# Performance work log

Hardware: AMD Instinct MI355X
Metric: run time of the kernel (lower is better)

Reference implementation:

```python
import jax, jax.numpy as jnp
import numpy as np

B, S, D, H, E, O = 8, 2048, 512, 8, 64, 512  # batch, seq, d_in, heads, head_dim, out_dim
NEG_INF = -1e9  # keras Attention adds -1e9 to masked scores


def setup_inputs() -> dict:
    key = jax.random.key(0)
    kq, kk, kv, ko, kx = jax.random.split(key, 5)
    # glorot-uniform-style scale for kernel_size=1 convs (fan_in=D, fan_out=E)
    sqkv = float(np.sqrt(6.0 / (D + E)))
    so = float(np.sqrt(6.0 / (H * E + O)))
    return {
        "query": jax.random.normal(kx, (B, S, D), dtype=jnp.float32),
        "Wq": jax.random.uniform(kq, (H, D, E), jnp.float32, -sqkv, sqkv),
        "Wk": jax.random.uniform(kk, (H, D, E), jnp.float32, -sqkv, sqkv),
        "Wv": jax.random.uniform(kv, (H, D, E), jnp.float32, -sqkv, sqkv),
        "Wo": jax.random.uniform(ko, (H * E, O), jnp.float32, -so, so),
    }


def reference(query, Wq, Wk, Wv, Wo):
    # value defaults to query (self-attention). Conv1D(kernel_size=1, no bias)
    # is a per-timestep linear map; all heads batched into one einsum.
    Q = jnp.einsum('bsd,hde->bhse', query, Wq)
    K = jnp.einsum('bsd,hde->bhse', query, Wk)
    V = jnp.einsum('bsd,hde->bhse', query, Wv)
    # keras Attention(use_scale=False, causal=True): scores = Q K^T (no scale)
    scores = jnp.einsum('bhse,bhte->bhst', Q, K)
    causal = jnp.tril(jnp.ones((S, S), dtype=bool))  # [S, S]
    scores = jnp.where(causal, scores, NEG_INF)
    attn = jax.nn.softmax(scores, axis=-1)
    ctx = jnp.einsum('bhst,bhte->bhse', attn, V)  # [B, H, S, E]
    # concat heads along last axis (head-major), then 1x1 conv projection
    ctx = ctx.transpose(0, 2, 1, 3).reshape(B, S, H * E)
    return jnp.einsum('bsf,fo->bso', ctx, Wo)
```

## Files before the change

kernel.cpp:

```cpp
#include <hip/hip_runtime.h>
#include <stdint.h>

#define Bb 8
#define Ss 2048
#define Dd 512
#define Hh 8
#define Ee 64
#define Oo 512
#define Ff 512
#define Ncat 1536

typedef _Float16 half_t;
typedef __attribute__((ext_vector_type(8))) _Float16 f16x8;
typedef __attribute__((ext_vector_type(4))) float f32x4;
typedef __attribute__((ext_vector_type(16))) float f32x16;
typedef __attribute__((ext_vector_type(4))) float f4;
typedef __attribute__((ext_vector_type(4))) half_t h16x4;
typedef __attribute__((ext_vector_type(4))) unsigned int u32x4;

__device__ __forceinline__ float exp2_fast(float x) {
    float r; asm("v_exp_f32 %0, %1" : "=v"(r) : "v"(x)); return r;
}
__device__ __forceinline__ f32x16 zero16() {
    f32x16 z;
#pragma unroll
    for (int i = 0; i < 16; ++i) z[i] = 0.f;
    return z;
}
__device__ __forceinline__ void gload16(const half_t* g, half_t* l) {
    __builtin_amdgcn_global_load_lds(
        (const __attribute__((address_space(1))) void*)g,
        (__attribute__((address_space(3))) void*)l, 16, 0, 0);
}

__global__ __launch_bounds__(256) void k_cvt_x(const float* __restrict__ x,
                                               half_t* __restrict__ xh) {
    int t = blockIdx.x * 256 + threadIdx.x;
    int s = t >> 6, c = t & 63;
    int cg = c >> 3, cl = c & 7;
    const float* src = x + (size_t)s * Dd + c * 8;
    f4 v0 = *(const f4*)src;
    f4 v1 = *(const f4*)(src + 4);
    union { half_t h[8]; u32x4 u; } o;
#pragma unroll
    for (int j = 0; j < 4; ++j) { o.h[j] = (half_t)v0[j]; o.h[4 + j] = (half_t)v1[j]; }
    int cd = cg * 8 + (cl ^ (s & 7));
    *(u32x4*)(xh + (size_t)s * Dd + cd * 8) = o.u;
}

__global__ __launch_bounds__(256) void k_cvt_w(const float* __restrict__ Wq, const float* __restrict__ Wk,
                                               const float* __restrict__ Wv, const float* __restrict__ Wo,
                                               half_t* __restrict__ Wcat, half_t* __restrict__ WoT) {
    int t = blockIdx.x * 256 + threadIdx.x;
    union { half_t h[8]; u32x4 u; } o;
    if (t < Ncat * 64) {
        int n = t >> 6, dc = t & 63;
        int sel = n >> 9, h = (n >> 6) & 7, e = n & 63;
        const float* W = (sel == 0) ? Wq : (sel == 1) ? Wk : Wv;
        const float* src = W + ((size_t)h * Dd + dc * 8) * Ee + e;
#pragma unroll
        for (int j = 0; j < 8; ++j) o.h[j] = (half_t)src[(size_t)j * Ee];
        int dcs = (dc & ~7) | ((dc & 7) ^ (n & 7));
        *(u32x4*)(Wcat + (size_t)n * Dd + dcs * 8) = o.u;
    } else {
        int u2 = t - Ncat * 64;
        int oo = u2 >> 6, fc = u2 & 63;
        const float* src = Wo + (size_t)(fc * 8) * Oo + oo;
#pragma unroll
        for (int j = 0; j < 8; ++j) o.h[j] = (half_t)src[(size_t)j * Oo];
        int fcs = (fc & ~7) | ((fc & 7) ^ (oo & 7));
        *(u32x4*)(WoT + (size_t)oo * Ff + fcs * 8) = o.u;
    }
}

__global__ __launch_bounds__(256, 2) void k_qkv(const half_t* __restrict__ A,
                                                const half_t* __restrict__ Bw,
                                                half_t* __restrict__ Q,
                                                half_t* __restrict__ K,
                                                half_t* __restrict__ Vt) {
    __shared__ __attribute__((aligned(16))) half_t Ab[2][128 * 64];
    __shared__ __attribute__((aligned(16))) half_t Bbuf[2][128 * 64];

    int bid = blockIdx.x;
    int virt = (bid & 7) * 192 + (bid >> 3);
    int bm = virt / 12, bn = virt % 12;
    int m0 = bm * 128, n0 = bn * 128;

    int wave = threadIdx.x >> 6, lane = threadIdx.x & 63;
    int ar = lane & 15, kg = lane >> 4;
    int wm = wave >> 1, wn = wave & 1;
    int lr = lane >> 3, lc = lane & 7;

    f32x4 acc[4][4];
#pragma unroll
    for (int i = 0; i < 4; ++i)
#pragma unroll
        for (int j = 0; j < 4; ++j) acc[i][j] = (f32x4){0, 0, 0, 0};

#define STAGE_QKV(buf, kt)                                                              \
    {                                                                                   \
        _Pragma("unroll")                                                               \
        for (int i = 0; i < 4; ++i) {                                                   \
            int seg = wave * 4 + i;                                                     \
            int row = seg * 8 + lr;                                                     \
            gload16(A  + (size_t)(m0 + row) * Dd + (kt) * 64 + lc * 8, &Ab[buf][seg * 512]);   \
            gload16(Bw + (size_t)(n0 + row) * Dd + (kt) * 64 + lc * 8, &Bbuf[buf][seg * 512]); \
        }                                                                               \
    }

    STAGE_QKV(0, 0);
    __syncthreads();
    int cur = 0;
    for (int kt = 0; kt < 8; ++kt) {
        if (kt < 7) STAGE_QKV(cur ^ 1, kt + 1);
        f16x8 bf[4][2];
#pragma unroll
        for (int n = 0; n < 4; ++n) {
            int row = wn * 64 + n * 16 + ar;
#pragma unroll
            for (int kh = 0; kh < 2; ++kh)
                bf[n][kh] = *(const f16x8*)&Bbuf[cur][row * 64 + (((kg + kh * 4)) ^ (row & 7)) * 8];
        }
#pragma unroll
        for (int mi = 0; mi < 4; ++mi) {
            int row = wm * 64 + mi * 16 + ar;
            f16x8 a0 = *(const f16x8*)&Ab[cur][row * 64 + ((kg)     ^ (row & 7)) * 8];
            f16x8 a1 = *(const f16x8*)&Ab[cur][row * 64 + ((kg + 4) ^ (row & 7)) * 8];
#pragma unroll
            for (int n = 0; n < 4; ++n) {
                acc[mi][n] = __builtin_amdgcn_mfma_f32_16x16x32_f16(a0, bf[n][0], acc[mi][n], 0, 0, 0);
                acc[mi][n] = __builtin_amdgcn_mfma_f32_16x16x32_f16(a1, bf[n][1], acc[mi][n], 0, 0, 0);
            }
        }
        __syncthreads();
        cur ^= 1;
    }
    int sel = n0 >> 9;
#pragma unroll
    for (int sn = 0; sn < 4; ++sn) {
        int nb = n0 + wn * 64 + sn * 16;
        int h = (nb >> 6) & 7, eb = nb & 63;
#pragma unroll
        for (int mi = 0; mi < 4; ++mi)
#pragma unroll
            for (int r = 0; r < 4; ++r) {
                int sg = m0 + wm * 64 + mi * 16 + kg * 4 + r;
                int bh = (sg >> 11) * 8 + h, sl = sg & 2047;
                half_t val = (half_t)acc[mi][sn][r];
                if (sel == 0)      Q [((size_t)bh * Ss + sl) * Ee + eb + ar] = val;
                else if (sel == 1) K [((size_t)bh * Ss + sl) * Ee + eb + ar] = val;
                else               Vt[((size_t)bh * Ee + eb + ar) * Ss + sl] = val;
            }
    }
#undef STAGE_QKV
}

__global__ __launch_bounds__(256, 4) void k_attn(const half_t* __restrict__ Q,
                                                 const half_t* __restrict__ Kg,
                                                 const half_t* __restrict__ Vtg,
                                                 half_t* __restrict__ ctx) {
    __shared__ __attribute__((aligned(16))) half_t Klds[2][32 * 64];
    __shared__ __attribute__((aligned(16))) half_t Vlds[2][64 * 32];

    int bid = blockIdx.x;
    int xcd = bid & 7;
    int idx = bid >> 3;
    int qb  = 15 - (idx >> 3);
    int bh  = xcd * 8 + (idx & 7);

    int wave = threadIdx.x >> 6, lane = threadIdx.x & 63;
    int ql = lane & 31, hi = lane >> 5;
    int qt32 = qb * 4 + wave;
    int ktmax = qb * 4 + 3;
    int qg = qt32 * 32 + ql;

    const half_t* Qb = Q   + (size_t)bh * Ss * Ee;
    const half_t* Kb = Kg  + (size_t)bh * Ss * Ee;
    const half_t* Vb = Vtg + (size_t)bh * Ee * Ss;

    const half_t* qp = Qb + (size_t)qg * Ee + hi * 8;
    f16x8 qf[4];
    const half_t l2e = (half_t)1.44269504f;
#pragma unroll
    for (int d = 0; d < 4; ++d) {
        qf[d] = *(const f16x8*)(qp + d * 16);
#pragma unroll
        for (int j = 0; j < 8; ++j) qf[d][j] *= l2e;
    }

    f32x16 ot0 = zero16(), ot1 = zero16();
    float m = -1e30f, lp = 0.f;

    const half_t* KbSrc = Kb + (size_t)(lane & 31) * Ee + (2 * wave + (lane >> 5)) * 8;
    const half_t* VbSrc = Vb + ((size_t)((wave >> 1) * 32 + (lane & 31))) * Ss
                             + (2 * (wave & 1) + (lane >> 5)) * 8;

#define STAGE_KV(buf, kt)                                            \
    {                                                                \
        gload16(KbSrc + (size_t)(kt) * 32 * Ee, &Klds[buf][wave * 512]); \
        gload16(VbSrc + (kt) * 32,              &Vlds[buf][wave * 512]); \
    }

    STAGE_KV(0, 0);
    int cur = 0;
    for (int kt = 0; kt <= ktmax; ++kt) {
        __syncthreads();
        if (kt < ktmax) STAGE_KV(cur ^ 1, kt + 1);
        if (kt <= qt32) {
            f16x8 kf0 = *(const f16x8*)&Klds[cur][lane * 8];
            f16x8 kf1 = *(const f16x8*)&Klds[cur][512 + lane * 8];
            f16x8 kf2 = *(const f16x8*)&Klds[cur][1024 + lane * 8];
            f16x8 kf3 = *(const f16x8*)&Klds[cur][1536 + lane * 8];

            f32x16 s = zero16();
            __builtin_amdgcn_s_setprio(1);
            s = __builtin_amdgcn_mfma_f32_32x32x16_f16(kf0, qf[0], s, 0, 0, 0);
            s = __builtin_amdgcn_mfma_f32_32x32x16_f16(kf1, qf[1], s, 0, 0, 0);
            s = __builtin_amdgcn_mfma_f32_32x32x16_f16(kf2, qf[2], s, 0, 0, 0);
            s = __builtin_amdgcn_mfma_f32_32x32x16_f16(kf3, qf[3], s, 0, 0, 0);
            __builtin_amdgcn_s_setprio(0);

            if (kt == qt32) {
#pragma unroll
                for (int r = 0; r < 16; ++r) {
                    int kloc = (r & 3) + 8 * (r >> 2) + 4 * hi;
                    if (kloc > ql) s[r] = -1e30f;
                }
            }

            float mt = s[0];
#pragma unroll
            for (int r = 1; r < 16; ++r) mt = fmaxf(mt, s[r]);
            mt = fmaxf(mt, __shfl_xor(mt, 32));
            if (!__all(mt <= m + 8.0f)) {
                float mn = fmaxf(m, mt);
                float sc = exp2_fast(m - mn);
#pragma unroll
                for (int r = 0; r < 16; ++r) { ot0[r] *= sc; ot1[r] *= sc; }
                lp *= sc;
                m = mn;
            }
            float rs = 0.f;
#pragma unroll
            for (int r = 0; r < 16; ++r) { s[r] = exp2_fast(s[r] - m); rs += s[r]; }
            lp += rs;

            unsigned w[8];
#pragma unroll
            for (int mm = 0; mm < 8; ++mm)
                asm("v_cvt_pkrtz_f16_f32 %0, %1, %2" : "=v"(w[mm]) : "v"(s[2 * mm]), "v"(s[2 * mm + 1]));
            unsigned t0 = (unsigned)__shfl_xor((int)(hi ? w[0] : w[2]), 32);
            unsigned t1 = (unsigned)__shfl_xor((int)(hi ? w[1] : w[3]), 32);
            unsigned t2 = (unsigned)__shfl_xor((int)(hi ? w[4] : w[6]), 32);
            unsigned t3 = (unsigned)__shfl_xor((int)(hi ? w[5] : w[7]), 32);
            union { unsigned u[4]; f16x8 v; } pb0, pb1;
            pb0.u[0] = hi ? t0 : w[0];  pb0.u[1] = hi ? t1 : w[1];
            pb0.u[2] = hi ? w[2] : t0;  pb0.u[3] = hi ? w[3] : t1;
            pb1.u[0] = hi ? t2 : w[4];  pb1.u[1] = hi ? t3 : w[5];
            pb1.u[2] = hi ? w[6] : t2;  pb1.u[3] = hi ? w[7] : t3;

            f16x8 va00 = *(const f16x8*)&Vlds[cur][lane * 8];
            f16x8 va01 = *(const f16x8*)&Vlds[cur][512 + lane * 8];
            f16x8 va10 = *(const f16x8*)&Vlds[cur][1024 + lane * 8];
            f16x8 va11 = *(const f16x8*)&Vlds[cur][1536 + lane * 8];

            __builtin_amdgcn_s_setprio(1);
            ot0 = __builtin_amdgcn_mfma_f32_32x32x16_f16(va00, pb0.v, ot0, 0, 0, 0);
            ot0 = __builtin_amdgcn_mfma_f32_32x32x16_f16(va01, pb1.v, ot0, 0, 0, 0);
            ot1 = __builtin_amdgcn_mfma_f32_32x32x16_f16(va10, pb0.v, ot1, 0, 0, 0);
            ot1 = __builtin_amdgcn_mfma_f32_32x32x16_f16(va11, pb1.v, ot1, 0, 0, 0);
            __builtin_amdgcn_s_setprio(0);
        }
        cur ^= 1;
    }
#undef STAGE_KV

    float lf = lp + __shfl_xor(lp, 32);
    float inv = 1.0f / lf;
    int b = bh >> 3, h = bh & 7;
    int qs = qg & 7;
    half_t* cb = ctx + ((size_t)b * Ss + qg) * Ff;
#pragma unroll
    for (int g = 0; g < 4; ++g) {
        h16x4 v0, v1;
#pragma unroll
        for (int j = 0; j < 4; ++j) {
            v0[j] = (half_t)(ot0[g * 4 + j] * inv);
            v1[j] = (half_t)(ot1[g * 4 + j] * inv);
        }
        *(h16x4*)(cb + (h * 8 + (g ^ qs)) * 8 + 4 * hi)       = v0;
        *(h16x4*)(cb + (h * 8 + ((g + 4) ^ qs)) * 8 + 4 * hi) = v1;
    }
}

__global__ __launch_bounds__(256, 2) void k_proj(const half_t* __restrict__ A,
                                                 const half_t* __restrict__ Bw,
                                                 float* __restrict__ out) {
    __shared__ __attribute__((aligned(16))) half_t Ab[2][128 * 64];
    __shared__ __attribute__((aligned(16))) half_t Bbuf[2][128 * 64];

    int bid = blockIdx.x;
    int virt = (bid & 7) * 64 + (bid >> 3);
    int bm = virt >> 2, bn = virt & 3;
    int m0 = bm * 128, n0 = bn * 128;

    int wave = threadIdx.x >> 6, lane = threadIdx.x & 63;
    int ar = lane & 15, kg = lane >> 4;
    int wm = wave >> 1, wn = wave & 1;
    int lr = lane >> 3, lc = lane & 7;

    f32x4 acc[4][4];
#pragma unroll
    for (int i = 0; i < 4; ++i)
#pragma unroll
        for (int j = 0; j < 4; ++j) acc[i][j] = (f32x4){0, 0, 0, 0};

#define STAGE_PRJ(buf, kt)                                                              \
    {                                                                                   \
        _Pragma("unroll")                                                               \
        for (int i = 0; i < 4; ++i) {                                                   \
            int seg = wave * 4 + i;                                                     \
            int row = seg * 8 + lr;                                                     \
            gload16(A  + (size_t)(m0 + row) * Ff + (kt) * 64 + lc * 8, &Ab[buf][seg * 512]);   \
            gload16(Bw + (size_t)(n0 + row) * Ff + (kt) * 64 + lc * 8, &Bbuf[buf][seg * 512]); \
        }                                                                               \
    }

    STAGE_PRJ(0, 0);
    __syncthreads();
    int cur = 0;
    for (int kt = 0; kt < 8; ++kt) {
        if (kt < 7) STAGE_PRJ(cur ^ 1, kt + 1);
        f16x8 bf[4][2];
#pragma unroll
        for (int n = 0; n < 4; ++n) {
            int row = wn * 64 + n * 16 + ar;
#pragma unroll
            for (int kh = 0; kh < 2; ++kh)
                bf[n][kh] = *(const f16x8*)&Bbuf[cur][row * 64 + (((kg + kh * 4)) ^ (row & 7)) * 8];
        }
#pragma unroll
        for (int mi = 0; mi < 4; ++mi) {
            int row = wm * 64 + mi * 16 + ar;
            f16x8 a0 = *(const f16x8*)&Ab[cur][row * 64 + ((kg)     ^ (row & 7)) * 8];
            f16x8 a1 = *(const f16x8*)&Ab[cur][row * 64 + ((kg + 4) ^ (row & 7)) * 8];
#pragma unroll
            for (int n = 0; n < 4; ++n) {
                acc[mi][n] = __builtin_amdgcn_mfma_f32_16x16x32_f16(a0, bf[n][0], acc[mi][n], 0, 0, 0);
                acc[mi][n] = __builtin_amdgcn_mfma_f32_16x16x32_f16(a1, bf[n][1], acc[mi][n], 0, 0, 0);
            }
        }
        __syncthreads();
        cur ^= 1;
    }
#pragma unroll
    for (int sn = 0; sn < 4; ++sn)
#pragma unroll
        for (int mi = 0; mi < 4; ++mi)
#pragma unroll
            for (int r = 0; r < 4; ++r) {
                int sg = m0 + wm * 64 + mi * 16 + kg * 4 + r;
                out[(size_t)sg * Oo + n0 + wn * 64 + sn * 16 + ar] = acc[mi][sn][r];
            }
#undef STAGE_PRJ
}

extern "C" void kernel_launch(void* const* d_in, const int* in_sizes, int n_in,
                              void* d_out, int out_size, void* d_ws, size_t ws_size,
                              hipStream_t stream) {
    const float* x  = (const float*)d_in[0];
    const float* Wq = (const float*)d_in[1];
    const float* Wk = (const float*)d_in[2];
    const float* Wv = (const float*)d_in[3];
    const float* Wo = (const float*)d_in[4];
    float* out = (float*)d_out;

    char* ws = (char*)d_ws;
    size_t off = 0;
    half_t* xh   = (half_t*)(ws + off); off += (size_t)Bb * Ss * Dd * 2;
    half_t* Wcat = (half_t*)(ws + off); off += (size_t)Ncat * Dd * 2;
    half_t* WoT  = (half_t*)(ws + off); off += (size_t)Oo * Ff * 2;
    half_t* Qd   = (half_t*)(ws + off); off += (size_t)Bb * Hh * Ss * Ee * 2;
    half_t* Kd   = (half_t*)(ws + off); off += (size_t)Bb * Hh * Ss * Ee * 2;
    half_t* Vtd  = (half_t*)(ws + off); off += (size_t)Bb * Hh * Ss * Ee * 2;
    half_t* ctx  = (half_t*)(ws + off); off += (size_t)Bb * Ss * Ff * 2;

    k_cvt_x<<<4096, 256, 0, stream>>>(x, xh);
    k_cvt_w<<<512, 256, 0, stream>>>(Wq, Wk, Wv, Wo, Wcat, WoT);
    k_qkv<<<1536, 256, 0, stream>>>(xh, Wcat, Qd, Kd, Vtd);
    k_attn<<<1024, 256, 0, stream>>>(Qd, Kd, Vtd, ctx);
    k_proj<<<512, 256, 0, stream>>>(ctx, WoT, out);
}
```

Measured before the change: 157.7 us.

## Stage 64-key tiles per barrier and reorder causal query-block dispatch

The attention kernel now stages 64 keys per double-buffer step instead of 32, doubling K/V LDS buffers and processing two 32-key subtiles per synchronization to halve barrier count. Query-block scheduling changes from strictly descending to an interleaved pattern to balance causal work across waves of blocks. The row-max reduction is rewritten as a tree for shorter dependency chains. It costs more LDS per block, which may reduce occupancy, and loads some keys that masked waves skip.

```diff
diff --git a/kernel.cpp b/kernel.cpp
--- a/kernel.cpp
+++ b/kernel.cpp
@@ -159,19 +159,26 @@
                                                  const half_t* __restrict__ Kg,
                                                  const half_t* __restrict__ Vtg,
                                                  half_t* __restrict__ ctx) {
-    __shared__ __attribute__((aligned(16))) half_t Klds[2][32 * 64];
-    __shared__ __attribute__((aligned(16))) half_t Vlds[2][64 * 32];
+    __shared__ __attribute__((aligned(16))) half_t Klds[2][64 * 64];
+    __shared__ __attribute__((aligned(16))) half_t Vlds[2][64 * 64];
 
     int bid = blockIdx.x;
     int xcd = bid & 7;
     int idx = bid >> 3;
-    int qb  = 15 - (idx >> 3);
+    int g   = idx >> 3;
+    int g0 = g & 3, j = g >> 2;
+    int qb;
+    switch (j) {
+        case 0:  qb = 15 - g0; break;
+        case 1:  qb = 8 + (g0 ^ 2); break;
+        case 2:  qb = 4 + g0; break;
+        default: qb = g0 ^ 1; break;
+    }
     int bh  = xcd * 8 + (idx & 7);
 
     int wave = threadIdx.x >> 6, lane = threadIdx.x & 63;
     int ql = lane & 31, hi = lane >> 5;
     int qt32 = qb * 4 + wave;
-    int ktmax = qb * 4 + 3;
     int qg = qt32 * 32 + ql;
 
     const half_t* Qb = Q   + (size_t)bh * Ss * Ee;
@@ -185,91 +192,106 @@
     for (int d = 0; d < 4; ++d) {
         qf[d] = *(const f16x8*)(qp + d * 16);
 #pragma unroll
-        for (int j = 0; j < 8; ++j) qf[d][j] *= l2e;
+        for (int jj = 0; jj < 8; ++jj) qf[d][jj] *= l2e;
     }
 
     f32x16 ot0 = zero16(), ot1 = zero16();
     float m = -1e30f, lp = 0.f;
 
-    const half_t* KbSrc = Kb + (size_t)(lane & 31) * Ee + (2 * wave + (lane >> 5)) * 8;
-    const half_t* VbSrc = Vb + ((size_t)((wave >> 1) * 32 + (lane & 31))) * Ss
-                             + (2 * (wave & 1) + (lane >> 5)) * 8;
-
-#define STAGE_KV(buf, kt)                                            \
-    {                                                                \
-        gload16(KbSrc + (size_t)(kt) * 32 * Ee, &Klds[buf][wave * 512]); \
-        gload16(VbSrc + (kt) * 32,              &Vlds[buf][wave * 512]); \
+#define STAGE_KV(buf, kt64)                                                                 \
+    {                                                                                       \
+        _Pragma("unroll")                                                                   \
+        for (int c = 0; c < 2; ++c) {                                                       \
+            int seg = 2 * wave + c;                                                         \
+            int tK = seg >> 2, dK = seg & 3;                                                \
+            gload16(Kb + ((size_t)(kt64) * 64 + tK * 32 + ql) * Ee + dK * 16 + hi * 8,      \
+                    &Klds[buf][seg * 512]);                                                 \
+            int eh = (seg >> 1) & 1, d2 = seg & 1;                                          \
+            gload16(Vb + (size_t)(eh * 32 + ql) * Ss + (kt64) * 64 + tK * 32 + d2 * 16 + hi * 8, \
+                    &Vlds[buf][seg * 512]);                                                 \
+        }                                                                                   \
     }
 
     STAGE_KV(0, 0);
     int cur = 0;
-    for (int kt = 0; kt <= ktmax; ++kt) {
+    int ktmax64 = qb * 2 + 1;
+    for (int kt64 = 0; kt64 <= ktmax64; ++kt64) {
         __syncthreads();
-        if (kt < ktmax) STAGE_KV(cur ^ 1, kt + 1);
-        if (kt <= qt32) {
-            f16x8 kf0 = *(const f16x8*)&Klds[cur][lane * 8];
-            f16x8 kf1 = *(const f16x8*)&Klds[cur][512 + lane * 8];
-            f16x8 kf2 = *(const f16x8*)&Klds[cur][1024 + lane * 8];
-            f16x8 kf3 = *(const f16x8*)&Klds[cur][1536 + lane * 8];
-
-            f32x16 s = zero16();
-            __builtin_amdgcn_s_setprio(1);
-            s = __builtin_amdgcn_mfma_f32_32x32x16_f16(kf0, qf[0], s, 0, 0, 0);
-            s = __builtin_amdgcn_mfma_f32_32x32x16_f16(kf1, qf[1], s, 0, 0, 0);
-            s = __builtin_amdgcn_mfma_f32_32x32x16_f16(kf2, qf[2], s, 0, 0, 0);
-            s = __builtin_amdgcn_mfma_f32_32x32x16_f16(kf3, qf[3], s, 0, 0, 0);
-            __builtin_amdgcn_s_setprio(0);
-
-            if (kt == qt32) {
-#pragma unroll
-                for (int r = 0; r < 16; ++r) {
-                    int kloc = (r & 3) + 8 * (r >> 2) + 4 * hi;
-                    if (kloc > ql) s[r] = -1e30f;
+        if (kt64 < ktmax64) STAGE_KV(cur ^ 1, kt64 + 1);
+#pragma unroll
+        for (int st = 0; st < 2; ++st) {
+            int kt32 = kt64 * 2 + st;
+            if (kt32 <= qt32) {
+                const half_t* Kbase = &Klds[cur][st * 2048];
+                const half_t* Vbase = &Vlds[cur][st * 2048];
+                f16x8 kf0 = *(const f16x8*)&Kbase[lane * 8];
+                f16x8 kf1 = *(const f16x8*)&Kbase[512 + lane * 8];
+                f16x8 kf2 = *(const f16x8*)&Kbase[1024 + lane * 8];
+                f16x8 kf3 = *(const f16x8*)&Kbase[1536 + lane * 8];
+
+                f32x16 s = zero16();
+                __builtin_amdgcn_s_setprio(1);
+                s = __builtin_amdgcn_mfma_f32_32x32x16_f16(kf0, qf[0], s, 0, 0, 0);
+                s = __builtin_amdgcn_mfma_f32_32x32x16_f16(kf1, qf[1], s, 0, 0, 0);
+                s = __builtin_amdgcn_mfma_f32_32x32x16_f16(kf2, qf[2], s, 0, 0, 0);
+                s = __builtin_amdgcn_mfma_f32_32x32x16_f16(kf3, qf[3], s, 0, 0, 0);
+                __builtin_amdgcn_s_setprio(0);
+
+                if (kt32 == qt32) {
+#pragma unroll
+                    for (int r = 0; r < 16; ++r) {
+                        int kloc = (r & 3) + 8 * (r >> 2) + 4 * hi;
+                        if (kloc > ql) s[r] = -1e30f;
+                    }
                 }
+
+                float m0a = fmaxf(s[0], s[1]),  m1a = fmaxf(s[2], s[3]);
+                float m2a = fmaxf(s[4], s[5]),  m3a = fmaxf(s[6], s[7]);
+                float m4a = fmaxf(s[8], s[9]),  m5a = fmaxf(s[10], s[11]);
+                float m6a = fmaxf(s[12], s[13]), m7a = fmaxf(s[14], s[15]);
+                float mb0 = fmaxf(fmaxf(m0a, m1a), fmaxf(m2a, m3a));
+                float mb1 = fmaxf(fmaxf(m4a, m5a), fmaxf(m6a, m7a));
+                float mt = fmaxf(mb0, mb1);
+                mt = fmaxf(mt, __shfl_xor(mt, 32));
+                if (!__all(mt <= m + 8.0f)) {
+                    float mn = fmaxf(m, mt);
+                    float sc = exp2_fast(m - mn);
+#pragma unroll
+                    for (int r = 0; r < 16; ++r) { ot0[r] *= sc; ot1[r] *= sc; }
+                    lp *= sc;
+                    m = mn;
+                }
+                float rs = 0.f;
+#pragma unroll
+                for (int r = 0; r < 16; ++r) { s[r] = exp2_fast(s[r] - m); rs += s[r]; }
+                lp += rs;
+
+                unsigned w[8];
+#pragma unroll
+                for (int mm = 0; mm < 8; ++mm)
+                    asm("v_cvt_pkrtz_f16_f32 %0, %1, %2" : "=v"(w[mm]) : "v"(s[2 * mm]), "v"(s[2 * mm + 1]));
+                unsigned t0 = (unsigned)__shfl_xor((int)(hi ? w[0] : w[2]), 32);
+                unsigned t1 = (unsigned)__shfl_xor((int)(hi ? w[1] : w[3]), 32);
+                unsigned t2 = (unsigned)__shfl_xor((int)(hi ? w[4] : w[6]), 32);
+                unsigned t3 = (unsigned)__shfl_xor((int)(hi ? w[5] : w[7]), 32);
+                union { unsigned u[4]; f16x8 v; } pb0, pb1;
+                pb0.u[0] = hi ? t0 : w[0];  pb0.u[1] = hi ? t1 : w[1];
+                pb0.u[2] = hi ? w[2] : t0;  pb0.u[3] = hi ? w[3] : t1;
+                pb1.u[0] = hi ? t2 : w[4];  pb1.u[1] = hi ? t3 : w[5];
+                pb1.u[2] = hi ? w[6] : t2;  pb1.u[3] = hi ? w[7] : t3;
+
+                f16x8 va00 = *(const f16x8*)&Vbase[lane * 8];
+                f16x8 va01 = *(const f16x8*)&Vbase[512 + lane * 8];
+                f16x8 va10 = *(const f16x8*)&Vbase[1024 + lane * 8];
+                f16x8 va11 = *(const f16x8*)&Vbase[1536 + lane * 8];
+
+                __builtin_amdgcn_s_setprio(1);
+                ot0 = __builtin_amdgcn_mfma_f32_32x32x16_f16(va00, pb0.v, ot0, 0, 0, 0);
+                ot0 = __builtin_amdgcn_mfma_f32_32x32x16_f16(va01, pb1.v, ot0, 0, 0, 0);
+                ot1 = __builtin_amdgcn_mfma_f32_32x32x16_f16(va10, pb0.v, ot1, 0, 0, 0);
+                ot1 = __builtin_amdgcn_mfma_f32_32x32x16_f16(va11, pb1.v, ot1, 0, 0, 0);
+                __builtin_amdgcn_s_setprio(0);
             }
-
-            float mt = s[0];
-#pragma unroll
-            for (int r = 1; r < 16; ++r) mt = fmaxf(mt, s[r]);
-            mt = fmaxf(mt, __shfl_xor(mt, 32));
-            if (!__all(mt <= m + 8.0f)) {
-                float mn = fmaxf(m, mt);
-                float sc = exp2_fast(m - mn);
-#pragma unroll
-                for (int r = 0; r < 16; ++r) { ot0[r] *= sc; ot1[r] *= sc; }
-                lp *= sc;
-                m = mn;
-            }
-            float rs = 0.f;
-#pragma unroll
-            for (int r = 0; r < 16; ++r) { s[r] = exp2_fast(s[r] - m); rs += s[r]; }
-            lp += rs;
-
-            unsigned w[8];
-#pragma unroll
-            for (int mm = 0; mm < 8; ++mm)
-                asm("v_cvt_pkrtz_f16_f32 %0, %1, %2" : "=v"(w[mm]) : "v"(s[2 * mm]), "v"(s[2 * mm + 1]));
-            unsigned t0 = (unsigned)__shfl_xor((int)(hi ? w[0] : w[2]), 32);
-            unsigned t1 = (unsigned)__shfl_xor((int)(hi ? w[1] : w[3]), 32);
-            unsigned t2 = (unsigned)__shfl_xor((int)(hi ? w[4] : w[6]), 32);
-            unsigned t3 = (unsigned)__shfl_xor((int)(hi ? w[5] : w[7]), 32);
-            union { unsigned u[4]; f16x8 v; } pb0, pb1;
-            pb0.u[0] = hi ? t0 : w[0];  pb0.u[1] = hi ? t1 : w[1];
-            pb0.u[2] = hi ? w[2] : t0;  pb0.u[3] = hi ? w[3] : t1;
-            pb1.u[0] = hi ? t2 : w[4];  pb1.u[1] = hi ? t3 : w[5];
-            pb1.u[2] = hi ? w[6] : t2;  pb1.u[3] = hi ? w[7] : t3;
-
-            f16x8 va00 = *(const f16x8*)&Vlds[cur][lane * 8];
-            f16x8 va01 = *(const f16x8*)&Vlds[cur][512 + lane * 8];
-            f16x8 va10 = *(const f16x8*)&Vlds[cur][1024 + lane * 8];
-            f16x8 va11 = *(const f16x8*)&Vlds[cur][1536 + lane * 8];
-
-            __builtin_amdgcn_s_setprio(1);
-            ot0 = __builtin_amdgcn_mfma_f32_32x32x16_f16(va00, pb0.v, ot0, 0, 0, 0);
-            ot0 = __builtin_amdgcn_mfma_f32_32x32x16_f16(va01, pb1.v, ot0, 0, 0, 0);
-            ot1 = __builtin_amdgcn_mfma_f32_32x32x16_f16(va10, pb0.v, ot1, 0, 0, 0);
-            ot1 = __builtin_amdgcn_mfma_f32_32x32x16_f16(va11, pb1.v, ot1, 0, 0, 0);
-            __builtin_amdgcn_s_setprio(0);
         }
         cur ^= 1;
     }
@@ -281,15 +303,15 @@
     int qs = qg & 7;
     half_t* cb = ctx + ((size_t)b * Ss + qg) * Ff;
 #pragma unroll
-    for (int g = 0; g < 4; ++g) {
+    for (int gg = 0; gg < 4; ++gg) {
         h16x4 v0, v1;
 #pragma unroll
-        for (int j = 0; j < 4; ++j) {
-            v0[j] = (half_t)(ot0[g * 4 + j] * inv);
-            v1[j] = (half_t)(ot1[g * 4 + j] * inv);
-        }
-        *(h16x4*)(cb + (h * 8 + (g ^ qs)) * 8 + 4 * hi)       = v0;
-        *(h16x4*)(cb + (h * 8 + ((g + 4) ^ qs)) * 8 + 4 * hi) = v1;
+        for (int jj = 0; jj < 4; ++jj) {
+            v0[jj] = (half_t)(ot0[gg * 4 + jj] * inv);
+            v1[jj] = (half_t)(ot1[gg * 4 + jj] * inv);
+        }
+        *(h16x4*)(cb + (h * 8 + (gg ^ qs)) * 8 + 4 * hi)       = v0;
+        *(h16x4*)(cb + (h * 8 + ((gg + 4) ^ qs)) * 8 + 4 * hi) = v1;
     }
 }
 
```

Result: faster. 152.6 us (-3.2%).
